# Performance work log

Measured on AMD Instinct MI355X. Metric: run time of the kernel, lower is better.

## Reference

```python
import jax, jax.numpy as jnp
import numpy as np

INV_DELTA = 15.0  # init kwarg inv_delta
EPS = 1e-12       # torch F.normalize eps


def setup_inputs() -> dict:
    key = jax.random.key(0)
    k1, k2 = jax.random.split(key)
    features = jax.random.normal(k1, (32, 256, 30, 30), dtype=jnp.float32)
    # _embedding buffer: randn clamped to >= 0
    embedding = jnp.maximum(jax.random.normal(k2, (2048, 256), dtype=jnp.float32), 0.0)
    # _min_distance_mean buffer, initialized to 0.5
    min_distance_mean = jnp.ones((1,), dtype=jnp.float32) * 0.5
    return {"features": features, "embedding": embedding,
            "min_distance_mean": min_distance_mean}


def reference(features, embedding, min_distance_mean):
    # crop 1-pixel border: [B,C,H,W] -> [B,C,H-2,W-2]
    f = features[:, :, 1:-1, 1:-1]
    # squared euclidean distance to each codeword via GEMM trick:
    # dist[b,k,h,w] = ||f[b,:,h,w]||^2 + ||e[k]||^2 - 2 <f, e[k]>
    f2 = jnp.sum(f * f, axis=1, keepdims=True)                 # [B,1,H',W']
    e2 = jnp.sum(embedding * embedding, axis=1)                # [K]
    xe = jnp.einsum('bchw,kc->bkhw', f, embedding)             # 1x1-conv GEMM
    dist = f2 + e2[None, :, None, None] - 2.0 * xe             # [B,K,H',W']
    # adaptive temperature softmax over codewords
    inv_delta_adaptive = INV_DELTA / min_distance_mean[0]
    codes = jax.nn.softmax(-inv_delta_adaptive * dist, axis=1)  # [B,K,H',W']
    # global average pool + L1 normalize
    bow = jnp.mean(codes, axis=(2, 3))                          # [B,K]
    bow = bow / jnp.maximum(jnp.sum(jnp.abs(bow), axis=1, keepdims=True), EPS)
    return (bow, codes)
```

## Files before the change

kernel.cpp:

```cpp
#include <hip/hip_runtime.h>
#include <hip/hip_bf16.h>
#include <math.h>

typedef __attribute__((ext_vector_type(8))) short bf16x8;
typedef __attribute__((ext_vector_type(16))) float f32x16;

#define B_ 32
#define C_ 256
#define K_ 2048
#define HW_ 784
#define NPIX 25088
#define FEAT_BSTRIDE 230400
#define FEAT_CSTRIDE 900
#define INV_DELTA 15.0f
#define LOG2E 1.4426950408889634f
#define QSCALE 409.6f
#define QDEC (LOG2E / QSCALE)

#define BM 128
#define BN 128
#define BKC 32
#define NCH 8
#define NSLAB 16

#define AS1 __attribute__((address_space(1)))
#define AS3 __attribute__((address_space(3)))

__device__ __forceinline__ ushort f2bf(float x) {
    __hip_bfloat16 h = __float2bfloat16(x);
    return *reinterpret_cast<ushort*>(&h);
}
__device__ __forceinline__ float bf2f(ushort u) {
    __hip_bfloat16 h;
    *reinterpret_cast<ushort*>(&h) = u;
    return __bfloat162float(h);
}
__device__ __forceinline__ void gl_lds16(const ushort* g, ushort* l) {
    __builtin_amdgcn_global_load_lds((AS1 const uint*)g, (AS3 uint*)l, 16, 0, 0);
}

__global__ void e2_kernel(const float* __restrict__ emb, float* __restrict__ e2) {
    int t = threadIdx.x;
    int wid = t >> 6, lane = t & 63;
    int k = blockIdx.x * 4 + wid;
    const float* er = emb + (size_t)k * C_;
    float v0 = er[lane], v1 = er[lane + 64], v2 = er[lane + 128], v3 = er[lane + 192];
    float s = v0 * v0 + v1 * v1 + v2 * v2 + v3 * v3;
#pragma unroll
    for (int off = 32; off > 0; off >>= 1) s += __shfl_xor(s, off);
    if (lane == 0) e2[k] = s;
}

__global__ void prep_e_kernel(const float* __restrict__ emb,
                              ushort* __restrict__ ehi, ushort* __restrict__ elo) {
    int i = blockIdx.x * 256 + threadIdx.x;
    float v = emb[i];
    ushort h = f2bf(v);
    float r = v - bf2f(h);
    ehi[i] = h;
    elo[i] = f2bf(r);
}

__global__ __launch_bounds__(256) void prep_f_kernel(const float* __restrict__ feat,
                                                     ushort* __restrict__ fhi,
                                                     ushort* __restrict__ flo) {
    __shared__ float F[256 * 65];
    int t = threadIdx.x;
    int px0 = blockIdx.x * 64;
    {
        int lane = t & 63, cq = t >> 6;
        int px = px0 + lane;
        int b = px / HW_, hw = px % HW_;
        int h = hw / 28, w = hw % 28;
        const float* base = feat + (size_t)b * FEAT_BSTRIDE + (size_t)(h + 1) * 30 + (w + 1);
#pragma unroll
        for (int cc = 0; cc < 64; ++cc) {
            int c = cq * 64 + cc;
            F[c * 65 + lane] = base[(size_t)c * FEAT_CSTRIDE];
        }
    }
    __syncthreads();
    {
        int px_l = t >> 2, cseg = t & 3;
        size_t ob = (size_t)(px0 + px_l) * C_ + cseg * 64;
        uint uh[32], ul[32];
#pragma unroll
        for (int j = 0; j < 32; ++j) {
            float v0 = F[(cseg * 64 + 2 * j) * 65 + px_l];
            float v1 = F[(cseg * 64 + 2 * j + 1) * 65 + px_l];
            ushort h0 = f2bf(v0), h1 = f2bf(v1);
            float r0 = v0 - bf2f(h0), r1 = v1 - bf2f(h1);
            uh[j] = (uint)h0 | ((uint)h1 << 16);
            ul[j] = (uint)f2bf(r0) | ((uint)f2bf(r1) << 16);
        }
#pragma unroll
        for (int j = 0; j < 8; ++j) {
            *reinterpret_cast<uint4*>(&fhi[ob + j * 8]) = *reinterpret_cast<uint4*>(&uh[j * 4]);
            *reinterpret_cast<uint4*>(&flo[ob + j * 8]) = *reinterpret_cast<uint4*>(&ul[j * 4]);
        }
    }
}

__global__ __launch_bounds__(256, 2) void gemm_kernel(
    const ushort* __restrict__ fhi, const ushort* __restrict__ flo,
    const ushort* __restrict__ ehi, const ushort* __restrict__ elo,
    const float* __restrict__ mdm, const float* __restrict__ e2g,
    ushort* __restrict__ zq, float* __restrict__ m_part, float* __restrict__ l_part)
{
    __shared__ __align__(16) ushort smem[2][4][BM * BKC];
    __shared__ float redA[2][132];
    __shared__ float redM[132];
    uint* zT = reinterpret_cast<uint*>(smem);

    int t = threadIdx.x;
    int lane = t & 63, wid = t >> 6;
    int wrow = wid >> 1, wcol = wid & 1;
    int g = lane >> 5, ci = lane & 31;

    int bid = blockIdx.x;
    int swz = (bid & 7) * 392 + (bid >> 3);
    int tile = swz >> 4, slab = swz & 15;
    int px0 = tile * BM;
    int k0 = slab * BN;

    auto stage = [&](int buf, int ch) {
        int c0 = ch * BKC;
#pragma unroll
        for (int i = 0; i < 2; ++i) {
            int p = t + i * 256;
            int rp = p >> 3, q = p & 7;
            int v = q ^ (rp & 7);
            int row = rp * 2 + (v >> 2);
            int cu = (v & 3) * 8;
            size_t ga = (size_t)(px0 + row) * C_ + c0 + cu;
            size_t gb = (size_t)(k0 + row) * C_ + c0 + cu;
            gl_lds16(fhi + ga, &smem[buf][0][p * 8]);
            gl_lds16(flo + ga, &smem[buf][1][p * 8]);
            gl_lds16(ehi + gb, &smem[buf][2][p * 8]);
            gl_lds16(elo + gb, &smem[buf][3][p * 8]);
        }
    };

    f32x16 acc[2][2];
#pragma unroll
    for (int mi = 0; mi < 2; ++mi)
#pragma unroll
        for (int ni = 0; ni < 2; ++ni)
            acc[mi][ni] = (f32x16)(0.0f);

    int xr = (ci >> 1) & 7;
    int bb4 = (ci & 1) * 4;
    int rpA0 = wrow * 32 + (ci >> 1);
    int rpB0 = wcol * 32 + (ci >> 1);

    stage(0, 0);
    __syncthreads();
    for (int ch = 0; ch < NCH; ++ch) {
        if (ch + 1 < NCH) stage((ch + 1) & 1, ch + 1);
        int cur = ch & 1;
#pragma unroll
        for (int s = 0; s < 2; ++s) {
            int qs = (bb4 + s * 2 + g) ^ xr;
            bf16x8 ah[2], av[2], bh[2], bv[2];
#pragma unroll
            for (int mi = 0; mi < 2; ++mi) {
                int off = (rpA0 + mi * 16) * 64 + qs * 8;
                ah[mi] = *reinterpret_cast<const bf16x8*>(&smem[cur][0][off]);
                av[mi] = *reinterpret_cast<const bf16x8*>(&smem[cur][1][off]);
            }
#pragma unroll
            for (int ni = 0; ni < 2; ++ni) {
                int off = (rpB0 + ni * 16) * 64 + qs * 8;
                bh[ni] = *reinterpret_cast<const bf16x8*>(&smem[cur][2][off]);
                bv[ni] = *reinterpret_cast<const bf16x8*>(&smem[cur][3][off]);
            }
#pragma unroll
            for (int mi = 0; mi < 2; ++mi)
#pragma unroll
                for (int ni = 0; ni < 2; ++ni) {
                    acc[mi][ni] = __builtin_amdgcn_mfma_f32_32x32x16_bf16(ah[mi], bh[ni], acc[mi][ni], 0, 0, 0);
                    acc[mi][ni] = __builtin_amdgcn_mfma_f32_32x32x16_bf16(ah[mi], bv[ni], acc[mi][ni], 0, 0, 0);
                    acc[mi][ni] = __builtin_amdgcn_mfma_f32_32x32x16_bf16(av[mi], bh[ni], acc[mi][ni], 0, 0, 0);
                }
        }
        __syncthreads();
    }

    const float alpha = INV_DELTA / mdm[0];
    float e2v[2];
#pragma unroll
    for (int ni = 0; ni < 2; ++ni) e2v[ni] = e2g[k0 + wcol * 64 + ni * 32 + ci];
#pragma unroll
    for (int mi = 0; mi < 2; ++mi)
#pragma unroll
        for (int ni = 0; ni < 2; ++ni)
            acc[mi][ni] = alpha * (2.0f * acc[mi][ni] - e2v[ni]);

    float ms[2][16];
    {
        float mt[2][16];
#pragma unroll
        for (int mi = 0; mi < 2; ++mi)
#pragma unroll
            for (int r = 0; r < 16; ++r)
                mt[mi][r] = fmaxf(acc[mi][0][r], acc[mi][1][r]);
#pragma unroll
        for (int off = 1; off < 32; off <<= 1)
#pragma unroll
            for (int mi = 0; mi < 2; ++mi)
#pragma unroll
                for (int r = 0; r < 16; ++r)
                    mt[mi][r] = fmaxf(mt[mi][r], __shfl_xor(mt[mi][r], off));
        if (ci == 0) {
#pragma unroll
            for (int mi = 0; mi < 2; ++mi)
#pragma unroll
                for (int r = 0; r < 16; ++r)
                    redA[wcol][wrow * 64 + mi * 32 + (r & 3) + 8 * (r >> 2) + 4 * g] = mt[mi][r];
        }
    }
    __syncthreads();
    if (t < 128) redM[t] = fmaxf(redA[0][t], redA[1][t]);
    __syncthreads();
#pragma unroll
    for (int mi = 0; mi < 2; ++mi)
#pragma unroll
        for (int r = 0; r < 16; ++r)
            ms[mi][r] = redM[wrow * 64 + mi * 32 + (r & 3) + 8 * (r >> 2) + 4 * g];

    {
        float lt[2][16];
#pragma unroll
        for (int mi = 0; mi < 2; ++mi)
#pragma unroll
            for (int r = 0; r < 16; ++r)
                lt[mi][r] = exp2f((acc[mi][0][r] - ms[mi][r]) * LOG2E) +
                            exp2f((acc[mi][1][r] - ms[mi][r]) * LOG2E);
#pragma unroll
        for (int off = 1; off < 32; off <<= 1)
#pragma unroll
            for (int mi = 0; mi < 2; ++mi)
#pragma unroll
                for (int r = 0; r < 16; ++r)
                    lt[mi][r] += __shfl_xor(lt[mi][r], off);
        if (ci == 0) {
#pragma unroll
            for (int mi = 0; mi < 2; ++mi)
#pragma unroll
                for (int r = 0; r < 16; ++r)
                    redA[wcol][wrow * 64 + mi * 32 + (r & 3) + 8 * (r >> 2) + 4 * g] = lt[mi][r];
        }
    }
    __syncthreads();
    if (t < 128) {
        m_part[(size_t)slab * NPIX + px0 + t] = redM[t];
        l_part[(size_t)slab * NPIX + px0 + t] = redA[0][t] + redA[1][t];
    }

#pragma unroll
    for (int mi = 0; mi < 2; ++mi)
#pragma unroll
        for (int ni = 0; ni < 2; ++ni) {
            int kl = wcol * 64 + ni * 32 + ci;
#pragma unroll
            for (int r = 0; r < 16; r += 2) {
                int row = wrow * 64 + mi * 32 + (r & 3) + 8 * (r >> 2) + 4 * g;
                float s0 = fmaxf((acc[mi][ni][r]     - ms[mi][r])     * QSCALE, -32760.f);
                float s1 = fmaxf((acc[mi][ni][r + 1] - ms[mi][r + 1]) * QSCALE, -32760.f);
                int q0 = (int)s0, q1 = (int)s1;
                uint u = ((uint)(ushort)(short)q0) | (((uint)(ushort)(short)q1) << 16);
                int pp = row >> 1;
                int seg = pp >> 2;
                zT[kl * 64 + ((seg ^ (kl & 15)) << 2) + (pp & 3)] = u;
            }
        }
    __syncthreads();

    const uint4* zT4 = reinterpret_cast<const uint4*>(zT);
#pragma unroll
    for (int it = 0; it < 8; ++it) {
        int kl = (t >> 4) + it * 16;
        int seg = t & 15;
        uint4 v = zT4[kl * 16 + (seg ^ (kl & 15))];
        int k = k0 + kl;
        int pxx = px0 + seg * 8;
        int bb = pxx / HW_, hh = pxx - bb * HW_;
        *reinterpret_cast<uint4*>(&zq[((size_t)bb * K_ + k) * HW_ + hh]) = v;
    }
}

__global__ void combine_kernel(const float* __restrict__ m_part, const float* __restrict__ l_part,
                               float* __restrict__ m_fin, float* __restrict__ rl_g) {
    int p = blockIdx.x * 256 + threadIdx.x;
    float m = -3.4e38f;
#pragma unroll
    for (int s = 0; s < NSLAB; ++s) m = fmaxf(m, m_part[(size_t)s * NPIX + p]);
    float l = 0.f;
#pragma unroll
    for (int s = 0; s < NSLAB; ++s)
        l += l_part[(size_t)s * NPIX + p] * exp2f((m_part[(size_t)s * NPIX + p] - m) * LOG2E);
    m_fin[p] = m;
    rl_g[p] = 1.0f / l;
}

__global__ __launch_bounds__(256) void finish_kernel(
    const ushort* __restrict__ zq, const float* __restrict__ m_part,
    const float* __restrict__ m_fin, const float* __restrict__ rl_g,
    float* __restrict__ codes, float* __restrict__ bow)
{
    __shared__ float corr[HW_], rls[HW_];
    __shared__ float bsum[64][4];
    int t = threadIdx.x;
    int kc = blockIdx.x, b = blockIdx.y;
    int slab = kc >> 1;
    for (int i = t; i < HW_; i += 256) {
        int p = b * HW_ + i;
        corr[i] = (m_part[(size_t)slab * NPIX + p] - m_fin[p]) * LOG2E;
        rls[i] = rl_g[p];
    }
    __syncthreads();
    int wid = t >> 6, lane = t & 63;
    for (int kl = 0; kl < 64; ++kl) {
        int k = kc * 64 + kl;
        size_t base = ((size_t)b * K_ + k) * HW_;
        float ssum = 0.f;
        if (t < 196) {
            uint2 raw = *reinterpret_cast<const uint2*>(&zq[base + t * 4]);
            int q0 = (int)(short)(raw.x & 0xffffu), q1 = (int)(short)(raw.x >> 16);
            int q2 = (int)(short)(raw.y & 0xffffu), q3 = (int)(short)(raw.y >> 16);
            float4 out;
            out.x = exp2f(fmaf((float)q0, QDEC, corr[t * 4 + 0])) * rls[t * 4 + 0];
            out.y = exp2f(fmaf((float)q1, QDEC, corr[t * 4 + 1])) * rls[t * 4 + 1];
            out.z = exp2f(fmaf((float)q2, QDEC, corr[t * 4 + 2])) * rls[t * 4 + 2];
            out.w = exp2f(fmaf((float)q3, QDEC, corr[t * 4 + 3])) * rls[t * 4 + 3];
            *reinterpret_cast<float4*>(&codes[base + t * 4]) = out;
            ssum = out.x + out.y + out.z + out.w;
        }
#pragma unroll
        for (int off = 32; off > 0; off >>= 1) ssum += __shfl_xor(ssum, off);
        if (lane == 0) bsum[kl][wid] = ssum;
    }
    __syncthreads();
    if (t < 64) {
        float s = bsum[t][0] + bsum[t][1] + bsum[t][2] + bsum[t][3];
        bow[(size_t)b * K_ + kc * 64 + t] = s * (1.0f / 784.0f);
    }
}

__global__ void bownorm_kernel(float* __restrict__ bow) {
    __shared__ float wred[4];
    __shared__ float denom_s;
    int b = blockIdx.x, t = threadIdx.x;
    float* row = bow + (size_t)b * K_;
    float v[8];
    float s = 0.f;
#pragma unroll
    for (int i = 0; i < 8; ++i) {
        v[i] = row[t + i * 256];
        s += fabsf(v[i]);
    }
#pragma unroll
    for (int off = 32; off > 0; off >>= 1) s += __shfl_xor(s, off);
    int wid = t >> 6, lane = t & 63;
    if (lane == 0) wred[wid] = s;
    __syncthreads();
    if (t == 0) denom_s = fmaxf(wred[0] + wred[1] + wred[2] + wred[3], 1e-12f);
    __syncthreads();
    float denom = denom_s;
#pragma unroll
    for (int i = 0; i < 8; ++i) row[t + i * 256] = v[i] / denom;
}

extern "C" void kernel_launch(void* const* d_in, const int* in_sizes, int n_in,
                              void* d_out, int out_size, void* d_ws, size_t ws_size,
                              hipStream_t stream) {
    const float* feat = (const float*)d_in[0];
    const float* emb  = (const float*)d_in[1];
    const float* mdm  = (const float*)d_in[2];
    float* bow   = (float*)d_out;
    float* codes = bow + (size_t)B_ * K_;

    char* ws = (char*)d_ws;
    size_t off = 0;
    auto alloc = [&](size_t bytes) { char* p = ws + off; off = (off + bytes + 255) & ~(size_t)255; return p; };
    ushort* ehi    = (ushort*)alloc((size_t)K_ * C_ * 2);
    ushort* elo    = (ushort*)alloc((size_t)K_ * C_ * 2);
    float*  e2     = (float*)alloc(K_ * 4);
    float*  m_part = (float*)alloc((size_t)NSLAB * NPIX * 4);
    float*  l_part = (float*)alloc((size_t)NSLAB * NPIX * 4);
    float*  m_fin  = (float*)alloc((size_t)NPIX * 4);
    float*  rl_g   = (float*)alloc((size_t)NPIX * 4);
    ushort* zq     = (ushort*)alloc((size_t)NPIX * K_ * 2);

    ushort* fhi = (ushort*)codes;
    ushort* flo = fhi + (size_t)NPIX * C_;

    e2_kernel<<<512, 256, 0, stream>>>(emb, e2);
    prep_e_kernel<<<2048, 256, 0, stream>>>(emb, ehi, elo);
    prep_f_kernel<<<392, 256, 0, stream>>>(feat, fhi, flo);
    gemm_kernel<<<3136, 256, 0, stream>>>(fhi, flo, ehi, elo, mdm, e2, zq, m_part, l_part);
    combine_kernel<<<98, 256, 0, stream>>>(m_part, l_part, m_fin, rl_g);
    finish_kernel<<<dim3(32, 32), 256, 0, stream>>>(zq, m_part, m_fin, rl_g, codes, bow);
    bownorm_kernel<<<32, 256, 0, stream>>>(bow);
}
```

Before: 236.5 us.

## Prefetch two chunks ahead and load fragments to registers before MFMA

The GEMM main loop now reads every LDS fragment of a chunk into registers before its MFMAs. A barrier after those reads lets the freed buffer be refilled with chunk ch+2 while the MFMAs run. Completion of global-to-LDS loads is tracked with explicit vmcnt waits, and wave priority is raised around the MFMA block. This hides more global load latency but raises register pressure and depends on hand-counted vmcnt values being correct.

```diff
diff --git a/kernel.cpp b/kernel.cpp
--- a/kernel.cpp
+++ b/kernel.cpp
@@ -154,36 +154,52 @@
     int rpB0 = wcol * 32 + (ci >> 1);
 
     stage(0, 0);
-    __syncthreads();
+    stage(1, 1);
+    asm volatile("s_waitcnt vmcnt(8)" ::: "memory");
+    __builtin_amdgcn_s_barrier();
+
     for (int ch = 0; ch < NCH; ++ch) {
-        if (ch + 1 < NCH) stage((ch + 1) & 1, ch + 1);
         int cur = ch & 1;
+        bf16x8 ah[2][2], av[2][2], bh[2][2], bv[2][2];
 #pragma unroll
         for (int s = 0; s < 2; ++s) {
             int qs = (bb4 + s * 2 + g) ^ xr;
-            bf16x8 ah[2], av[2], bh[2], bv[2];
 #pragma unroll
             for (int mi = 0; mi < 2; ++mi) {
                 int off = (rpA0 + mi * 16) * 64 + qs * 8;
-                ah[mi] = *reinterpret_cast<const bf16x8*>(&smem[cur][0][off]);
-                av[mi] = *reinterpret_cast<const bf16x8*>(&smem[cur][1][off]);
+                ah[s][mi] = *reinterpret_cast<const bf16x8*>(&smem[cur][0][off]);
+                av[s][mi] = *reinterpret_cast<const bf16x8*>(&smem[cur][1][off]);
             }
 #pragma unroll
             for (int ni = 0; ni < 2; ++ni) {
                 int off = (rpB0 + ni * 16) * 64 + qs * 8;
-                bh[ni] = *reinterpret_cast<const bf16x8*>(&smem[cur][2][off]);
-                bv[ni] = *reinterpret_cast<const bf16x8*>(&smem[cur][3][off]);
+                bh[s][ni] = *reinterpret_cast<const bf16x8*>(&smem[cur][2][off]);
+                bv[s][ni] = *reinterpret_cast<const bf16x8*>(&smem[cur][3][off]);
             }
+        }
+        asm volatile("s_waitcnt lgkmcnt(0)" ::: "memory");
+        __builtin_amdgcn_sched_barrier(0);
+        __builtin_amdgcn_s_barrier();
+        if (ch + 2 < NCH) stage(cur, ch + 2);
+        __builtin_amdgcn_sched_barrier(0);
+        __builtin_amdgcn_s_setprio(1);
+#pragma unroll
+        for (int s = 0; s < 2; ++s)
 #pragma unroll
             for (int mi = 0; mi < 2; ++mi)
 #pragma unroll
                 for (int ni = 0; ni < 2; ++ni) {
-                    acc[mi][ni] = __builtin_amdgcn_mfma_f32_32x32x16_bf16(ah[mi], bh[ni], acc[mi][ni], 0, 0, 0);
-                    acc[mi][ni] = __builtin_amdgcn_mfma_f32_32x32x16_bf16(ah[mi], bv[ni], acc[mi][ni], 0, 0, 0);
-                    acc[mi][ni] = __builtin_amdgcn_mfma_f32_32x32x16_bf16(av[mi], bh[ni], acc[mi][ni], 0, 0, 0);
+                    acc[mi][ni] = __builtin_amdgcn_mfma_f32_32x32x16_bf16(ah[s][mi], bh[s][ni], acc[mi][ni], 0, 0, 0);
+                    acc[mi][ni] = __builtin_amdgcn_mfma_f32_32x32x16_bf16(ah[s][mi], bv[s][ni], acc[mi][ni], 0, 0, 0);
+                    acc[mi][ni] = __builtin_amdgcn_mfma_f32_32x32x16_bf16(av[s][mi], bh[s][ni], acc[mi][ni], 0, 0, 0);
                 }
-        }
-        __syncthreads();
+        __builtin_amdgcn_s_setprio(0);
+        if (ch + 2 < NCH) {
+            asm volatile("s_waitcnt vmcnt(8)" ::: "memory");
+        } else {
+            asm volatile("s_waitcnt vmcnt(0)" ::: "memory");
+        }
+        __builtin_amdgcn_s_barrier();
     }
 
     const float alpha = INV_DELTA / mdm[0];
```

After: 236.7 us. Within noise of the previous version (+0.1%).

## Load embedding operand directly into registers, halve LDS, raise occupancy

Applied to the files above, without the earlier changes.

The B (embedding hi/lo) operand is no longer staged through LDS. Each lane loads its bf16x8 fragments straight from global memory into double-buffered registers, with a prefetch one sub-step ahead. This halves the shared-memory footprint and lifts the occupancy hint from 2 to 3 blocks per CU. Synchronisation switches to manual vmcnt waits plus raw barriers, which relies on exact counts of outstanding loads. Register pressure rises and the B global loads are uncoalesced per lane (32-byte chunks from strided rows).

```diff
diff --git a/kernel.cpp b/kernel.cpp
--- a/kernel.cpp
+++ b/kernel.cpp
@@ -101,16 +101,16 @@
     }
 }
 
-__global__ __launch_bounds__(256, 2) void gemm_kernel(
+__global__ __launch_bounds__(256, 3) void gemm_kernel(
     const ushort* __restrict__ fhi, const ushort* __restrict__ flo,
     const ushort* __restrict__ ehi, const ushort* __restrict__ elo,
     const float* __restrict__ mdm, const float* __restrict__ e2g,
     ushort* __restrict__ zq, float* __restrict__ m_part, float* __restrict__ l_part)
 {
-    __shared__ __align__(16) ushort smem[2][4][BM * BKC];
+    __shared__ __align__(16) ushort Asmem[2][2][BM * BKC];
     __shared__ float redA[2][132];
     __shared__ float redM[132];
-    uint* zT = reinterpret_cast<uint*>(smem);
+    uint* zT = reinterpret_cast<uint*>(Asmem);
 
     int t = threadIdx.x;
     int lane = t & 63, wid = t >> 6;
@@ -123,7 +123,7 @@
     int px0 = tile * BM;
     int k0 = slab * BN;
 
-    auto stage = [&](int buf, int ch) {
+    auto stageA = [&](int buf, int ch) {
         int c0 = ch * BKC;
 #pragma unroll
         for (int i = 0; i < 2; ++i) {
@@ -133,11 +133,26 @@
             int row = rp * 2 + (v >> 2);
             int cu = (v & 3) * 8;
             size_t ga = (size_t)(px0 + row) * C_ + c0 + cu;
-            size_t gb = (size_t)(k0 + row) * C_ + c0 + cu;
-            gl_lds16(fhi + ga, &smem[buf][0][p * 8]);
-            gl_lds16(flo + ga, &smem[buf][1][p * 8]);
-            gl_lds16(ehi + gb, &smem[buf][2][p * 8]);
-            gl_lds16(elo + gb, &smem[buf][3][p * 8]);
+            gl_lds16(fhi + ga, &Asmem[buf][0][p * 8]);
+            gl_lds16(flo + ga, &Asmem[buf][1][p * 8]);
+        }
+    };
+
+    const ushort* pbh[2];
+    const ushort* pbl[2];
+#pragma unroll
+    for (int ni = 0; ni < 2; ++ni) {
+        size_t r = (size_t)(k0 + wcol * 64 + ni * 32 + ci) * C_ + g * 8;
+        pbh[ni] = ehi + r;
+        pbl[ni] = elo + r;
+    }
+    bf16x8 bhS[2][2], bvS[2][2];
+    auto loadB = [&](int slot, int gs) {
+        int off = gs * 16;
+#pragma unroll
+        for (int ni = 0; ni < 2; ++ni) {
+            bhS[slot][ni] = *reinterpret_cast<const bf16x8*>(pbh[ni] + off);
+            bvS[slot][ni] = *reinterpret_cast<const bf16x8*>(pbl[ni] + off);
         }
     };
 
@@ -151,39 +166,42 @@
     int xr = (ci >> 1) & 7;
     int bb4 = (ci & 1) * 4;
     int rpA0 = wrow * 32 + (ci >> 1);
-    int rpB0 = wcol * 32 + (ci >> 1);
-
-    stage(0, 0);
-    __syncthreads();
+
+    stageA(0, 0);
+    loadB(0, 0);
+    asm volatile("s_waitcnt vmcnt(4)" ::: "memory");
+    __builtin_amdgcn_s_barrier();
+
+#pragma unroll
     for (int ch = 0; ch < NCH; ++ch) {
-        if (ch + 1 < NCH) stage((ch + 1) & 1, ch + 1);
-        int cur = ch & 1;
+        if (ch + 1 < NCH) stageA((ch + 1) & 1, ch + 1);
 #pragma unroll
         for (int s = 0; s < 2; ++s) {
+            int gs = ch * 2 + s;
+            if (gs + 1 < 2 * NCH) loadB((gs + 1) & 1, gs + 1);
+            __builtin_amdgcn_sched_barrier(0);
             int qs = (bb4 + s * 2 + g) ^ xr;
-            bf16x8 ah[2], av[2], bh[2], bv[2];
+            bf16x8 ah[2], av[2];
 #pragma unroll
             for (int mi = 0; mi < 2; ++mi) {
                 int off = (rpA0 + mi * 16) * 64 + qs * 8;
-                ah[mi] = *reinterpret_cast<const bf16x8*>(&smem[cur][0][off]);
-                av[mi] = *reinterpret_cast<const bf16x8*>(&smem[cur][1][off]);
+                ah[mi] = *reinterpret_cast<const bf16x8*>(&Asmem[ch & 1][0][off]);
+                av[mi] = *reinterpret_cast<const bf16x8*>(&Asmem[ch & 1][1][off]);
             }
-#pragma unroll
-            for (int ni = 0; ni < 2; ++ni) {
-                int off = (rpB0 + ni * 16) * 64 + qs * 8;
-                bh[ni] = *reinterpret_cast<const bf16x8*>(&smem[cur][2][off]);
-                bv[ni] = *reinterpret_cast<const bf16x8*>(&smem[cur][3][off]);
-            }
+            int cs = gs & 1;
 #pragma unroll
             for (int mi = 0; mi < 2; ++mi)
 #pragma unroll
                 for (int ni = 0; ni < 2; ++ni) {
-                    acc[mi][ni] = __builtin_amdgcn_mfma_f32_32x32x16_bf16(ah[mi], bh[ni], acc[mi][ni], 0, 0, 0);
-                    acc[mi][ni] = __builtin_amdgcn_mfma_f32_32x32x16_bf16(ah[mi], bv[ni], acc[mi][ni], 0, 0, 0);
-                    acc[mi][ni] = __builtin_amdgcn_mfma_f32_32x32x16_bf16(av[mi], bh[ni], acc[mi][ni], 0, 0, 0);
+                    acc[mi][ni] = __builtin_amdgcn_mfma_f32_32x32x16_bf16(ah[mi], bhS[cs][ni], acc[mi][ni], 0, 0, 0);
+                    acc[mi][ni] = __builtin_amdgcn_mfma_f32_32x32x16_bf16(ah[mi], bvS[cs][ni], acc[mi][ni], 0, 0, 0);
+                    acc[mi][ni] = __builtin_amdgcn_mfma_f32_32x32x16_bf16(av[mi], bhS[cs][ni], acc[mi][ni], 0, 0, 0);
                 }
         }
-        __syncthreads();
+        if (ch + 1 < NCH) {
+            asm volatile("s_waitcnt vmcnt(4)" ::: "memory");
+            __builtin_amdgcn_s_barrier();
+        }
     }
 
     const float alpha = INV_DELTA / mdm[0];
```

New measurement: 233.4 us. About the same (-1.3%).
